# Kernel tuning notes

Measured on AMD Instinct MI355X. Metric: run time of the kernel, lower is better.

Reference implementation:

```python
import jax, jax.numpy as jnp
import numpy as np

B, S, D = 2, 2048, 2048
H, HK = 16, 4          # n_heads, n_kv_heads
DK = D // H            # 128
REP = H // HK


def setup_inputs() -> dict:
    key = jax.random.key(0)
    ks = jax.random.split(key, 9)
    x = jax.random.normal(ks[0], (B, S, D), dtype=jnp.float32)
    # RoPE tables: [max_seq_len, d_k/2]
    inv_freq = 1.0 / (10000.0 ** (jnp.arange(0, DK, 2, dtype=jnp.float32) / DK))
    t = jnp.arange(S, dtype=jnp.float32)
    freqs = jnp.outer(t, inv_freq)  # [S, DK/2]
    freqs_cos = jnp.cos(freqs)
    freqs_sin = jnp.sin(freqs)
    sc = 0.02
    return {
        "x": x,
        "freqs_cos": freqs_cos,
        "freqs_sin": freqs_sin,
        "wq_w": jax.random.normal(ks[1], (D, D), dtype=jnp.float32) * sc,
        "wq_b": jnp.zeros((D,), dtype=jnp.float32),
        "wk_w": jax.random.normal(ks[2], (HK * DK, D), dtype=jnp.float32) * sc,
        "wk_b": jnp.zeros((HK * DK,), dtype=jnp.float32),
        "wv_w": jax.random.normal(ks[3], (HK * DK, D), dtype=jnp.float32) * sc,
        "wv_b": jnp.zeros((HK * DK,), dtype=jnp.float32),
        "wo_w": jax.random.normal(ks[4], (D, D), dtype=jnp.float32) * sc,
        "wo_b": jnp.zeros((D,), dtype=jnp.float32),
    }


def _apply_rope(t, cos, sin):
    # t: [b, h, s, dk]; cos/sin: [1, 1, s, dk/2]; interleaved pairs (even=real, odd=imag)
    tr = t[..., 0::2]
    ti = t[..., 1::2]
    out_r = tr * cos - ti * sin
    out_i = tr * sin + ti * cos
    return jnp.stack([out_r, out_i], axis=-1).reshape(t.shape)


def reference(x, freqs_cos, freqs_sin, wq_w, wq_b, wk_w, wk_b, wv_w, wv_b, wo_w, wo_b):
    b, s, d = x.shape
    q = (x @ wq_w.T + wq_b).reshape(b, s, H, DK).transpose(0, 2, 1, 3)   # [b,H,s,dk]
    k = (x @ wk_w.T + wk_b).reshape(b, s, HK, DK).transpose(0, 2, 1, 3)  # [b,HK,s,dk]
    v = (x @ wv_w.T + wv_b).reshape(b, s, HK, DK).transpose(0, 2, 1, 3)

    cos = freqs_cos[:s][None, None]  # [1,1,s,dk/2]
    sin = freqs_sin[:s][None, None]
    q = _apply_rope(q, cos, sin)
    k = _apply_rope(k, cos, sin)

    # GQA: group q heads by kv head instead of materializing repeat_kv
    qg = q.reshape(b, HK, REP, s, DK)
    scores = jnp.einsum("bgrqd,bgkd->bgrqk", qg, k) / jnp.sqrt(jnp.float32(DK))
    causal = jnp.triu(jnp.full((s, s), -jnp.inf, dtype=scores.dtype), k=1)
    attn = jax.nn.softmax(scores + causal, axis=-1)  # dropout=0.0 -> no-op
    out = jnp.einsum("bgrqk,bgkd->bgrqd", attn, v)   # [b,HK,REP,s,dk]
    out = out.reshape(b, H, s, DK).transpose(0, 2, 1, 3).reshape(b, s, d)
    return out @ wo_w.T + wo_b
```

## Files before the change

kernel.cpp:

```cpp
#include <hip/hip_runtime.h>

#define BDIM 2
#define SDIM 2048
#define DDIM 2048
#define HQ 16
#define HKV 4
#define DKH 128
#define NKV 512
#define NQKV 3072
#define MROWS 4096

typedef __attribute__((ext_vector_type(8))) short bf16x8;
typedef __attribute__((ext_vector_type(4))) float f32x4;
typedef __attribute__((ext_vector_type(8))) unsigned short u16x8;
typedef __attribute__((ext_vector_type(4))) unsigned short u16x4;

#define AS1 __attribute__((address_space(1)))
#define AS3 __attribute__((address_space(3)))

__device__ __forceinline__ unsigned short f2bf(float f) {
    union { float f; unsigned int u; } v; v.f = f;
    unsigned int r = v.u + 0x7FFFu + ((v.u >> 16) & 1u);
    return (unsigned short)(r >> 16);
}
__device__ __forceinline__ float bf2f(unsigned short u) {
    union { unsigned int u; float f; } v; v.u = ((unsigned int)u) << 16;
    return v.f;
}
__device__ __forceinline__ unsigned int pack2bf(float a, float b) {
    return (unsigned int)f2bf(a) | ((unsigned int)f2bf(b) << 16);
}

#define NX   ((size_t)MROWS * DDIM)
#define NWQ  ((size_t)DDIM * DDIM)
#define NWKV ((size_t)NKV * DDIM)
#define CAST_BLOCKS 18432
__global__ void cast_all(const float* __restrict__ x, const float* __restrict__ wq,
                         const float* __restrict__ wk, const float* __restrict__ wv,
                         const float* __restrict__ wo, unsigned short* __restrict__ dst,
                         const float* __restrict__ qb, const float* __restrict__ kb,
                         const float* __restrict__ vb, float* __restrict__ b3) {
    if (blockIdx.x >= CAST_BLOCKS) {
        int i = (blockIdx.x - CAST_BLOCKS) * 256 + threadIdx.x;
        if (i < DDIM) b3[i] = qb[i];
        else if (i < DDIM + NKV) b3[i] = kb[i - DDIM];
        else if (i < NQKV) b3[i] = vb[i - DDIM - NKV];
        return;
    }
    size_t i = ((size_t)blockIdx.x * blockDim.x + threadIdx.x) * 4;
    const size_t N0 = NX, N1 = N0 + NWQ, N2 = N1 + NWKV, N3 = N2 + NWKV;
    const float* src; size_t off;
    if (i < N0)      { src = x;  off = i; }
    else if (i < N1) { src = wq; off = i - N0; }
    else if (i < N2) { src = wk; off = i - N1; }
    else if (i < N3) { src = wv; off = i - N2; }
    else             { src = wo; off = i - N3; }
    float4 v = *(const float4*)(src + off);
    u16x4 o;
    o[0] = f2bf(v.x); o[1] = f2bf(v.y); o[2] = f2bf(v.z); o[3] = f2bf(v.w);
    *(u16x4*)(dst + i) = o;
}

__global__ void rope_trans(unsigned short* __restrict__ buf,
                           const float* __restrict__ cosT, const float* __restrict__ sinT,
                           unsigned short* __restrict__ Vt, float qscale) {
    if (blockIdx.x < MROWS) {
        int r = blockIdx.x, pos = r & (SDIM - 1);
        int col0 = threadIdx.x * 8;
        unsigned short* p = buf + (size_t)r * NQKV + col0;
        int i0 = (col0 & 127) >> 1;
        float4 c4 = *(const float4*)(cosT + pos * 64 + i0);
        float4 s4 = *(const float4*)(sinT + pos * 64 + i0);
        float sc = (col0 < DDIM) ? qscale : 1.f;
        u16x8 v = *(const u16x8*)p;
        u16x8 o;
        float cc[4] = {c4.x, c4.y, c4.z, c4.w}, ss[4] = {s4.x, s4.y, s4.z, s4.w};
#pragma unroll
        for (int k = 0; k < 4; ++k) {
            float xr = bf2f(v[2 * k]), xi = bf2f(v[2 * k + 1]);
            o[2 * k]     = f2bf((xr * cc[k] - xi * ss[k]) * sc);
            o[2 * k + 1] = f2bf((xr * ss[k] + xi * cc[k]) * sc);
        }
        *(u16x8*)p = o;
    } else {
        __shared__ unsigned short T[32][33];
        if (threadIdx.x >= 256) return;
        int t = blockIdx.x - MROWS;
        int s0 = (t & 63) * 32, d0 = ((t >> 6) & 15) * 32, b = t >> 10;
        int c = threadIdx.x & 31, r4 = threadIdx.x >> 5;
        for (int rr = r4; rr < 32; rr += 8)
            T[rr][c] = buf[(size_t)(b * SDIM + s0 + rr) * NQKV + (DDIM + NKV) + d0 + c];
        __syncthreads();
        int cp = ((c & 0x0C) << 1) | ((c & 0x10) >> 2) | (c & 3);
        for (int rr = r4; rr < 32; rr += 8)
            Vt[(size_t)(b * NKV + d0 + rr) * SDIM + s0 + cp] = T[c][rr];
    }
}

template <int BF16OUT>
__global__ __launch_bounds__(256) void gemm_bt(
    const unsigned short* __restrict__ A,
    const unsigned short* __restrict__ Bm,
    const float* __restrict__ bias,
    void* __restrict__ Cv,
    int pitch, int Kdim) {
    __shared__ unsigned short As[128 * 32];
    __shared__ unsigned short Bs[128 * 32];
    const int tid = threadIdx.x;
    const int w = tid >> 6, lane = tid & 63;
    const int ml = lane & 15, quad = lane >> 4;
    const int m0 = blockIdx.y * 128, n0 = blockIdx.x * 128;
    const int wr = (w >> 1) * 64, wc = (w & 1) * 64;
    const int swz = ((quad ^ (ml & 3) ^ ((ml >> 2) & 3))) * 8;

    f32x4 acc[4][4] = {};

    const int c0 = tid, c1 = tid + 256;
    const int ar0 = c0 >> 2, ar1 = c1 >> 2;
    const int ak0 = ((c0 & 3) ^ ((c0 >> 2) & 3) ^ ((c0 >> 4) & 3)) * 8;
    const int ak1 = ((c1 & 3) ^ ((c1 >> 2) & 3) ^ ((c1 >> 4) & 3)) * 8;

    for (int kt = 0; kt < Kdim; kt += 32) {
        __builtin_amdgcn_global_load_lds(
            (const AS1 unsigned int*)(A + (size_t)(m0 + ar0) * Kdim + kt + ak0),
            (AS3 unsigned int*)(As + c0 * 8), 16, 0, 0);
        __builtin_amdgcn_global_load_lds(
            (const AS1 unsigned int*)(A + (size_t)(m0 + ar1) * Kdim + kt + ak1),
            (AS3 unsigned int*)(As + c1 * 8), 16, 0, 0);
        __builtin_amdgcn_global_load_lds(
            (const AS1 unsigned int*)(Bm + (size_t)(n0 + ar0) * Kdim + kt + ak0),
            (AS3 unsigned int*)(Bs + c0 * 8), 16, 0, 0);
        __builtin_amdgcn_global_load_lds(
            (const AS1 unsigned int*)(Bm + (size_t)(n0 + ar1) * Kdim + kt + ak1),
            (AS3 unsigned int*)(Bs + c1 * 8), 16, 0, 0);
        __syncthreads();

        bf16x8 af[4], bfr[4];
#pragma unroll
        for (int i = 0; i < 4; ++i)
            af[i] = *(const bf16x8*)&As[(wr + i * 16 + ml) * 32 + swz];
#pragma unroll
        for (int j = 0; j < 4; ++j)
            bfr[j] = *(const bf16x8*)&Bs[(wc + j * 16 + ml) * 32 + swz];
#pragma unroll
        for (int i = 0; i < 4; ++i)
#pragma unroll
            for (int j = 0; j < 4; ++j)
                acc[i][j] = __builtin_amdgcn_mfma_f32_16x16x32_bf16(af[i], bfr[j], acc[i][j], 0, 0, 0);
        __syncthreads();
    }

#pragma unroll
    for (int j = 0; j < 4; ++j) {
        int col = n0 + wc + j * 16 + ml;
        float bj = bias[col];
#pragma unroll
        for (int i = 0; i < 4; ++i) {
            int row0 = m0 + wr + i * 16 + quad * 4;
#pragma unroll
            for (int r = 0; r < 4; ++r) {
                float v = acc[i][j][r] + bj;
                if (BF16OUT)
                    ((unsigned short*)Cv)[(size_t)(row0 + r) * pitch + col] = f2bf(v);
                else
                    ((float*)Cv)[(size_t)(row0 + r) * pitch + col] = v;
            }
        }
    }
}

__global__ __launch_bounds__(256, 2) void attn_fwd(
    const unsigned short* __restrict__ Qp,
    const unsigned short* __restrict__ Kp,
    const unsigned short* __restrict__ Vt,
    unsigned short* __restrict__ O) {
    const int l = blockIdx.x;
    const int j = l >> 5;
    const int h = l & 15;
    const int b = (l >> 4) & 1;
    const int g = h >> 2;
    const int tid = threadIdx.x;
    const int w = tid >> 6, lane = tid & 63;
    const int ml = lane & 15, quad = lane >> 4;
    const int rsub = lane >> 2, seg = lane & 3;

    __shared__ unsigned short Ks[4 * 64 * 32];
    __shared__ unsigned short Vs[2 * 128 * 32];

    const bool low_pair = ((w < 2) != (l & 1));
    const int myqt = low_pair ? j : (31 - j);
    const int q0 = myqt * 64 + (w & 1) * 32;
    const int ktend = 32 - j;

    bf16x8 aq[2][4];
#pragma unroll
    for (int g2 = 0; g2 < 2; ++g2) {
        const size_t qrow = (size_t)(b * SDIM + q0 + g2 * 16 + ml);
#pragma unroll
        for (int kc = 0; kc < 4; ++kc)
            aq[g2][kc] = *(const bf16x8*)(Qp + qrow * NQKV + h * DKH + kc * 32 + quad * 8);
    }

    f32x4 o_acc[2][8] = {};
    float l_acc[2] = {0.f, 0.f};

    for (int kt = 0; kt < ktend; ++kt) {
        const int kb = kt * 64;
        __syncthreads();
#pragma unroll
        for (int kc = 0; kc < 4; ++kc)
            __builtin_amdgcn_global_load_lds(
                (const AS1 unsigned int*)(Kp + (size_t)(b * SDIM + kb + w * 16 + rsub) * NQKV + g * DKH + kc * 32 + seg * 8),
                (AS3 unsigned int*)(Ks + kc * 2048 + w * 512 + lane * 8), 16, 0, 0);
#pragma unroll
        for (int c = 0; c < 4; ++c) {
            int u = w * 4 + c, kc2 = u >> 3, rg = u & 7;
            __builtin_amdgcn_global_load_lds(
                (const AS1 unsigned int*)(Vt + (size_t)(b * NKV + g * DKH + rg * 16 + rsub) * SDIM + kb + kc2 * 32 + seg * 8),
                (AS3 unsigned int*)(Vs + u * 512 + lane * 8), 16, 0, 0);
        }
        __syncthreads();

        if (kb <= q0 + 31) {
            f32x4 st[2][4];
#pragma unroll
            for (int t = 0; t < 4; ++t) {
                bf16x8 ak[4];
#pragma unroll
                for (int kc = 0; kc < 4; ++kc)
                    ak[kc] = *(const bf16x8*)&Ks[kc * 2048 + (t * 16 + ml) * 32 + quad * 8];
#pragma unroll
                for (int g2 = 0; g2 < 2; ++g2) {
                    f32x4 sc = {};
#pragma unroll
                    for (int kc = 0; kc < 4; ++kc)
                        sc = __builtin_amdgcn_mfma_f32_16x16x32_bf16(ak[kc], aq[g2][kc], sc, 0, 0, 0);
                    st[g2][t] = sc;
                }
            }

            if (kb + 63 > q0) {
#pragma unroll
                for (int g2 = 0; g2 < 2; ++g2) {
                    int qg = q0 + g2 * 16 + ml;
#pragma unroll
                    for (int t = 0; t < 4; ++t) {
                        int kvb = kb + t * 16 + quad * 4;
#pragma unroll
                        for (int r = 0; r < 4; ++r)
                            if (kvb + r > qg) st[g2][t][r] = -INFINITY;
                    }
                }
            }

            unsigned int pk[2][4][2];
#pragma unroll
            for (int g2 = 0; g2 < 2; ++g2) {
#pragma unroll
                for (int t = 0; t < 4; ++t) {
                    float p0 = __expf(st[g2][t][0] - 20.f);
                    float p1 = __expf(st[g2][t][1] - 20.f);
                    float p2 = __expf(st[g2][t][2] - 20.f);
                    float p3 = __expf(st[g2][t][3] - 20.f);
                    l_acc[g2] += (p0 + p1) + (p2 + p3);
                    pk[g2][t][0] = pack2bf(p0, p1);
                    pk[g2][t][1] = pack2bf(p2, p3);
                }
            }

#pragma unroll
            for (int c = 0; c < 2; ++c) {
                union { unsigned int u[4]; bf16x8 v; } pb[2];
#pragma unroll
                for (int g2 = 0; g2 < 2; ++g2) {
                    pb[g2].u[0] = pk[g2][2 * c][0];     pb[g2].u[1] = pk[g2][2 * c][1];
                    pb[g2].u[2] = pk[g2][2 * c + 1][0]; pb[g2].u[3] = pk[g2][2 * c + 1][1];
                }
#pragma unroll
                for (int dt = 0; dt < 8; ++dt) {
                    bf16x8 av = *(const bf16x8*)&Vs[c * 4096 + (dt * 16 + ml) * 32 + quad * 8];
                    o_acc[0][dt] = __builtin_amdgcn_mfma_f32_16x16x32_bf16(av, pb[0].v, o_acc[0][dt], 0, 0, 0);
                    o_acc[1][dt] = __builtin_amdgcn_mfma_f32_16x16x32_bf16(av, pb[1].v, o_acc[1][dt], 0, 0, 0);
                }
            }
        }
    }

#pragma unroll
    for (int g2 = 0; g2 < 2; ++g2) {
        float lt = l_acc[g2];
        lt += __shfl_xor(lt, 16);
        lt += __shfl_xor(lt, 32);
        float inv = 1.f / lt;
        size_t rowbase = (size_t)(b * SDIM + q0 + g2 * 16 + ml) * DDIM + h * DKH + quad * 4;
#pragma unroll
        for (int dt = 0; dt < 8; ++dt) {
            u16x4 ov;
#pragma unroll
            for (int r = 0; r < 4; ++r)
                ov[r] = f2bf(o_acc[g2][dt][r] * inv);
            *(u16x4*)(O + rowbase + dt * 16) = ov;
        }
    }
}

extern "C" void kernel_launch(void* const* d_in, const int* in_sizes, int n_in,
                              void* d_out, int out_size, void* d_ws, size_t ws_size,
                              hipStream_t stream) {
    const float* x    = (const float*)d_in[0];
    const float* fcos = (const float*)d_in[1];
    const float* fsin = (const float*)d_in[2];
    const float* wq_w = (const float*)d_in[3];
    const float* wq_b = (const float*)d_in[4];
    const float* wk_w = (const float*)d_in[5];
    const float* wk_b = (const float*)d_in[6];
    const float* wv_w = (const float*)d_in[7];
    const float* wv_b = (const float*)d_in[8];
    const float* wo_w = (const float*)d_in[9];
    const float* wo_b = (const float*)d_in[10];
    float* out = (float*)d_out;

    char* ws = (char*)d_ws;
    size_t off = 0;
    auto alloc = [&](size_t bytes) {
        char* p = ws + off;
        off += (bytes + 255) & ~(size_t)255;
        return p;
    };
    unsigned short* xb  = (unsigned short*)alloc(NX * 2);
    unsigned short* W3  = (unsigned short*)alloc((size_t)NQKV * DDIM * 2);
    unsigned short* wob = (unsigned short*)alloc(NWQ * 2);
    float* b3           = (float*)alloc((size_t)NQKV * 4);
    unsigned short* qkv = (unsigned short*)alloc((size_t)MROWS * NQKV * 2);
    unsigned short* Vt  = (unsigned short*)alloc((size_t)BDIM * NKV * SDIM * 2);
    unsigned short* att = (unsigned short*)alloc((size_t)MROWS * DDIM * 2);

    cast_all<<<dim3(CAST_BLOCKS + 12), dim3(256), 0, stream>>>(
        x, wq_w, wk_w, wv_w, wo_w, xb, wq_b, wk_b, wv_b, b3);

    gemm_bt<1><<<dim3(NQKV / 128, MROWS / 128), 256, 0, stream>>>(xb, W3, b3, qkv, NQKV, DDIM);

    const float scale = 0.08838834764831845f;
    rope_trans<<<dim3(MROWS + 2048), dim3(320), 0, stream>>>(qkv, fcos, fsin, Vt, scale);

    attn_fwd<<<dim3(512), dim3(256), 0, stream>>>(qkv, qkv + DDIM, Vt, att);

    gemm_bt<0><<<dim3(DDIM / 128, MROWS / 128), 256, 0, stream>>>(att, wob, wo_b, out, DDIM, DDIM);
}
```

Before: 321.6 us.

## Replace GEMM with 256x256 double-buffered 8-wave pipelined kernel; remap attention blocks

Replaces the 128x128 single-buffered GEMM with a 256x256-tile, 512-thread kernel that uses a K-step of 64, double-buffered LDS, and staged async global-to-LDS loads interleaved with MFMA phases, plus raised wave priority around the MFMAs. The goal is to hide memory latency and raise data reuse in the QKV and output projections. The attention kernel's block-to-(batch, head, q-tile) mapping is also changed so the two batches pair q tiles in reverse order, which should balance the causal workload. The larger tiles use much more LDS (64KB) and yield fewer blocks (192 and 128), which risks under-filling the CUs.

```diff
diff --git a/kernel.cpp b/kernel.cpp
--- a/kernel.cpp
+++ b/kernel.cpp
@@ -98,72 +98,125 @@
 }
 
 template <int BF16OUT>
-__global__ __launch_bounds__(256) void gemm_bt(
+__global__ __launch_bounds__(512, 2) void gemm8(
     const unsigned short* __restrict__ A,
     const unsigned short* __restrict__ Bm,
     const float* __restrict__ bias,
     void* __restrict__ Cv,
     int pitch, int Kdim) {
-    __shared__ unsigned short As[128 * 32];
-    __shared__ unsigned short Bs[128 * 32];
+    __shared__ unsigned short As[2][2][8192];
+    __shared__ unsigned short Bs[2][2][8192];
+
     const int tid = threadIdx.x;
-    const int w = tid >> 6, lane = tid & 63;
+    const int lane = tid & 63;
+    const int wid = tid >> 6;
     const int ml = lane & 15, quad = lane >> 4;
-    const int m0 = blockIdx.y * 128, n0 = blockIdx.x * 128;
-    const int wr = (w >> 1) * 64, wc = (w & 1) * 64;
-    const int swz = ((quad ^ (ml & 3) ^ ((ml >> 2) & 3))) * 8;
-
-    f32x4 acc[4][4] = {};
-
-    const int c0 = tid, c1 = tid + 256;
-    const int ar0 = c0 >> 2, ar1 = c1 >> 2;
-    const int ak0 = ((c0 & 3) ^ ((c0 >> 2) & 3) ^ ((c0 >> 4) & 3)) * 8;
-    const int ak1 = ((c1 & 3) ^ ((c1 >> 2) & 3) ^ ((c1 >> 4) & 3)) * 8;
-
-    for (int kt = 0; kt < Kdim; kt += 32) {
-        __builtin_amdgcn_global_load_lds(
-            (const AS1 unsigned int*)(A + (size_t)(m0 + ar0) * Kdim + kt + ak0),
-            (AS3 unsigned int*)(As + c0 * 8), 16, 0, 0);
-        __builtin_amdgcn_global_load_lds(
-            (const AS1 unsigned int*)(A + (size_t)(m0 + ar1) * Kdim + kt + ak1),
-            (AS3 unsigned int*)(As + c1 * 8), 16, 0, 0);
-        __builtin_amdgcn_global_load_lds(
-            (const AS1 unsigned int*)(Bm + (size_t)(n0 + ar0) * Kdim + kt + ak0),
-            (AS3 unsigned int*)(Bs + c0 * 8), 16, 0, 0);
-        __builtin_amdgcn_global_load_lds(
-            (const AS1 unsigned int*)(Bm + (size_t)(n0 + ar1) * Kdim + kt + ak1),
-            (AS3 unsigned int*)(Bs + c1 * 8), 16, 0, 0);
-        __syncthreads();
-
-        bf16x8 af[4], bfr[4];
-#pragma unroll
-        for (int i = 0; i < 4; ++i)
-            af[i] = *(const bf16x8*)&As[(wr + i * 16 + ml) * 32 + swz];
-#pragma unroll
-        for (int j = 0; j < 4; ++j)
-            bfr[j] = *(const bf16x8*)&Bs[(wc + j * 16 + ml) * 32 + swz];
-#pragma unroll
-        for (int i = 0; i < 4; ++i)
-#pragma unroll
-            for (int j = 0; j < 4; ++j)
-                acc[i][j] = __builtin_amdgcn_mfma_f32_16x16x32_bf16(af[i], bfr[j], acc[i][j], 0, 0, 0);
-        __syncthreads();
-    }
-
-#pragma unroll
-    for (int j = 0; j < 4; ++j) {
-        int col = n0 + wc + j * 16 + ml;
-        float bj = bias[col];
-#pragma unroll
-        for (int i = 0; i < 4; ++i) {
-            int row0 = m0 + wr + i * 16 + quad * 4;
-#pragma unroll
-            for (int r = 0; r < 4; ++r) {
-                float v = acc[i][j][r] + bj;
+    const int wm = wid >> 2, wn = wid & 3;
+    const int bhf = wn >> 1;
+    const int brb = (wn & 1) * 64;
+    const int m0 = blockIdx.y * 256, n0 = blockIdx.x * 256;
+    const int NT = Kdim >> 6;
+    const int xr = ml & 7;
+
+    const int sr = tid >> 3;
+    const int sk = ((tid & 7) ^ (sr & 7)) * 8;
+    const unsigned short* Ag0 = A + (size_t)(m0 + sr) * Kdim + sk;
+    const unsigned short* Bg0 = Bm + (size_t)(n0 + sr) * Kdim + sk;
+    const size_t rk64 = (size_t)64 * Kdim;
+
+    f32x4 acc[8][4] = {};
+
+#define STG_A(bf, hf, kt)                                                                       \
+    do {                                                                                        \
+        __builtin_amdgcn_global_load_lds(                                                       \
+            (const AS1 unsigned int*)(Ag0 + (size_t)(hf) * 2 * rk64 + (kt)),                    \
+            (AS3 unsigned int*)(&As[bf][hf][tid * 8]), 16, 0, 0);                               \
+        __builtin_amdgcn_global_load_lds(                                                       \
+            (const AS1 unsigned int*)(Ag0 + (size_t)(hf) * 2 * rk64 + rk64 + (kt)),             \
+            (AS3 unsigned int*)(&As[bf][hf][4096 + tid * 8]), 16, 0, 0);                        \
+    } while (0)
+#define STG_B(bf, hf, kt)                                                                       \
+    do {                                                                                        \
+        __builtin_amdgcn_global_load_lds(                                                       \
+            (const AS1 unsigned int*)(Bg0 + (size_t)(hf) * 2 * rk64 + (kt)),                    \
+            (AS3 unsigned int*)(&Bs[bf][hf][tid * 8]), 16, 0, 0);                               \
+        __builtin_amdgcn_global_load_lds(                                                       \
+            (const AS1 unsigned int*)(Bg0 + (size_t)(hf) * 2 * rk64 + rk64 + (kt)),             \
+            (AS3 unsigned int*)(&Bs[bf][hf][4096 + tid * 8]), 16, 0, 0);                        \
+    } while (0)
+
+    STG_B(0, 0, 0); STG_B(0, 1, 0);
+    STG_A(0, 0, 0); STG_A(0, 1, 0);
+    if (NT > 1) {
+        STG_B(1, 0, 64); STG_B(1, 1, 64);
+        asm volatile("s_waitcnt vmcnt(4)" ::: "memory");
+    } else {
+        asm volatile("s_waitcnt vmcnt(0)" ::: "memory");
+    }
+    __builtin_amdgcn_s_barrier();
+
+    for (int G = 0; G < NT; ++G) {
+        const int cur = G & 1, nxt = cur ^ 1;
+        const int ktA = (G + 1) * 64, ktB = (G + 2) * 64;
+        const unsigned short* Ah = As[cur][wm];
+        const unsigned short* Bh = Bs[cur][bhf];
+
+        bf16x8 bfr[4][2];
+#pragma unroll
+        for (int nj = 0; nj < 4; ++nj)
+#pragma unroll
+            for (int kk = 0; kk < 2; ++kk)
+                bfr[nj][kk] = *(const bf16x8*)&Bh[(brb + nj * 16 + ml) * 64 + ((kk * 4 + quad) ^ xr) * 8];
+
+#pragma unroll
+        for (int p = 0; p < 4; ++p) {
+            bf16x8 af[2][2];
+#pragma unroll
+            for (int mi = 0; mi < 2; ++mi)
+#pragma unroll
+                for (int kk = 0; kk < 2; ++kk)
+                    af[mi][kk] = *(const bf16x8*)&Ah[((p * 2 + mi) * 16 + ml) * 64 + ((kk * 4 + quad) ^ xr) * 8];
+
+            if (p == 0)      { if (G + 1 < NT) STG_A(nxt, 0, ktA); }
+            else if (p == 1) { if (G + 1 < NT) STG_A(nxt, 1, ktA); }
+            else if (p == 2) { if (G + 2 < NT) STG_B(cur, 0, ktB); }
+            else             { if (G + 2 < NT) STG_B(cur, 1, ktB); }
+
+            __builtin_amdgcn_s_barrier();
+            __builtin_amdgcn_s_setprio(1);
+#pragma unroll
+            for (int kk = 0; kk < 2; ++kk)
+#pragma unroll
+                for (int mi = 0; mi < 2; ++mi)
+#pragma unroll
+                    for (int nj = 0; nj < 4; ++nj)
+                        acc[p * 2 + mi][nj] = __builtin_amdgcn_mfma_f32_16x16x32_bf16(
+                            af[mi][kk], bfr[nj][kk], acc[p * 2 + mi][nj], 0, 0, 0);
+            __builtin_amdgcn_s_setprio(0);
+            if (p == 3) {
+                if (G < NT - 2)       { asm volatile("s_waitcnt vmcnt(4)" ::: "memory"); }
+                else if (G == NT - 2) { asm volatile("s_waitcnt vmcnt(0)" ::: "memory"); }
+            }
+            __builtin_amdgcn_s_barrier();
+        }
+    }
+#undef STG_A
+#undef STG_B
+
+#pragma unroll
+    for (int nj = 0; nj < 4; ++nj) {
+        const int col = n0 + wn * 64 + nj * 16 + ml;
+        const float bj = bias[col];
+#pragma unroll
+        for (int mi = 0; mi < 8; ++mi) {
+            const int row0 = m0 + wm * 128 + mi * 16 + quad * 4;
+#pragma unroll
+            for (int rr = 0; rr < 4; ++rr) {
+                float v = acc[mi][nj][rr] + bj;
                 if (BF16OUT)
-                    ((unsigned short*)Cv)[(size_t)(row0 + r) * pitch + col] = f2bf(v);
+                    ((unsigned short*)Cv)[(size_t)(row0 + rr) * pitch + col] = f2bf(v);
                 else
-                    ((float*)Cv)[(size_t)(row0 + r) * pitch + col] = v;
+                    ((float*)Cv)[(size_t)(row0 + rr) * pitch + col] = v;
             }
         }
     }
@@ -175,9 +228,11 @@
     const unsigned short* __restrict__ Vt,
     unsigned short* __restrict__ O) {
     const int l = blockIdx.x;
-    const int j = l >> 5;
-    const int h = l & 15;
-    const int b = (l >> 4) & 1;
+    const int idx = l & 255, layer = l >> 8;
+    const int jb = idx & 15;
+    const int j = layer ? (15 - jb) : jb;
+    const int h = idx >> 4;
+    const int b = layer;
     const int g = h >> 2;
     const int tid = threadIdx.x;
     const int w = tid >> 6, lane = tid & 63;
@@ -338,12 +393,12 @@
     cast_all<<<dim3(CAST_BLOCKS + 12), dim3(256), 0, stream>>>(
         x, wq_w, wk_w, wv_w, wo_w, xb, wq_b, wk_b, wv_b, b3);
 
-    gemm_bt<1><<<dim3(NQKV / 128, MROWS / 128), 256, 0, stream>>>(xb, W3, b3, qkv, NQKV, DDIM);
+    gemm8<1><<<dim3(NQKV / 256, MROWS / 256), 512, 0, stream>>>(xb, W3, b3, qkv, NQKV, DDIM);
 
     const float scale = 0.08838834764831845f;
     rope_trans<<<dim3(MROWS + 2048), dim3(320), 0, stream>>>(qkv, fcos, fsin, Vt, scale);
 
     attn_fwd<<<dim3(512), dim3(256), 0, stream>>>(qkv, qkv + DDIM, Vt, att);
 
-    gemm_bt<0><<<dim3(DDIM / 128, MROWS / 128), 256, 0, stream>>>(att, wob, wo_b, out, DDIM, DDIM);
-}
+    gemm8<0><<<dim3(DDIM / 256, MROWS / 256), 512, 0, stream>>>(att, wob, wo_b, out, DDIM, DDIM);
+}
```

New measurement: 326.2 us. About the same (+1.4%).
